# Optimization experiments

Hardware: AMD Instinct MI355X
Metric: run time of the kernel (lower is better)

Reference implementation:

```python
import jax, jax.numpy as jnp
import numpy as np
import math

D = 256      # d_model
NH = 8       # n_heads
NP = 8       # n_points
HW = 200     # H = W
N = HW * HW  # 40000 tokens
B = 1
DH = D // NH # head dim = 32


def _offset_bias():
    # replicates torch _reset_parameters grid_init bias for sampling_offsets
    thetas = np.arange(NH, dtype=np.float32) * (2.0 * np.pi / NH)
    g = np.stack([np.cos(thetas), np.sin(thetas)], -1)
    g = g / np.abs(g).max(-1, keepdims=True)
    g = np.tile(g[:, None, :], (1, NP, 1)) * np.arange(1, NP + 1, dtype=np.float32)[None, :, None]
    return jnp.asarray(g.reshape(-1), dtype=jnp.float32)


def _xavier(key, fan_in, fan_out):
    lim = math.sqrt(6.0 / (fan_in + fan_out))
    return jax.random.uniform(key, (fan_in, fan_out), jnp.float32, -lim, lim)


def setup_inputs() -> dict:
    key = jax.random.key(0)
    ks = jax.random.split(key, 6)
    return {
        "query": jax.random.normal(ks[0], (B, N, D), jnp.float32),
        "value": jax.random.normal(ks[1], (B, N, D), jnp.float32),
        "reference_points": jax.random.uniform(ks[2], (B, N, 2), jnp.float32),
        # weights stored as (in, out); torch Linear computes x @ W.T + b
        "W_off": jnp.zeros((D, NH * NP * 2), jnp.float32),   # torch init: zeros
        "b_off": _offset_bias(),
        "W_attn": jnp.zeros((D, NH * NP), jnp.float32),      # torch init: zeros
        "b_attn": jnp.zeros((NH * NP,), jnp.float32),
        "W_val": _xavier(ks[3], D, D),
        "b_val": jnp.zeros((D,), jnp.float32),
        "W_out": _xavier(ks[4], D, D),
        "b_out": jnp.zeros((D,), jnp.float32),
    }


def _grid_sample(value_h, locs):
    """Bilinear grid_sample, align_corners=False, zero padding.

    value_h: (B, NH, Hi, Wi, DH) per-head value map
    locs:    (B, N, NH, NP, 2) sampling locations in [0,1], last dim (x, y)
    returns: (B, N, NH, NP, DH)
    """
    Bb, Hh, Hi, Wi, Dh = value_h.shape
    g = locs * 2.0 - 1.0                                  # grid in [-1, 1]
    x = ((g[..., 0] + 1.0) * Wi - 1.0) * 0.5              # pixel coords (B,N,NH,NP)
    y = ((g[..., 1] + 1.0) * Hi - 1.0) * 0.5
    x0f, y0f = jnp.floor(x), jnp.floor(y)
    wx, wy = x - x0f, y - y0f
    x0, y0 = x0f.astype(jnp.int32), y0f.astype(jnp.int32)
    x1, y1 = x0 + 1, y0 + 1

    vflat = value_h.reshape(Bb, Hh, Hi * Wi, Dh)

    def corner(yi, xi, w):
        valid = (yi >= 0) & (yi < Hi) & (xi >= 0) & (xi < Wi)
        yc = jnp.clip(yi, 0, Hi - 1)
        xc = jnp.clip(xi, 0, Wi - 1)
        flat = yc * Wi + xc                               # (B,N,NH,NP)
        idx = jnp.transpose(flat, (0, 2, 1, 3)).reshape(Bb, Hh, -1)
        gathered = jnp.take_along_axis(vflat, idx[..., None], axis=2)  # (B,NH,N*NP,DH)
        wm = (w * valid.astype(w.dtype))
        wm = jnp.transpose(wm, (0, 2, 1, 3)).reshape(Bb, Hh, -1)
        return gathered * wm[..., None]

    out = (corner(y0, x0, (1.0 - wx) * (1.0 - wy))
           + corner(y0, x1, wx * (1.0 - wy))
           + corner(y1, x0, (1.0 - wx) * wy)
           + corner(y1, x1, wx * wy))                     # (B,NH,N*NP,DH)
    out = out.reshape(Bb, Hh, -1, NP, Dh)                 # (B,NH,N,NP,DH)
    return jnp.transpose(out, (0, 2, 1, 3, 4))            # (B,N,NH,NP,DH)


def reference(query, value, reference_points, W_off, b_off, W_attn, b_attn, W_val, b_val, W_out, b_out):
    Bb, Nn, C = query.shape
    H = W = int(math.sqrt(Nn))

    offsets = (query @ W_off + b_off).reshape(Bb, Nn, NH, NP, 2)
    attn = jax.nn.softmax((query @ W_attn + b_attn).reshape(Bb, Nn, NH, NP), axis=-1)

    locs = reference_points[:, :, None, None, :] + offsets / H
    locs = jnp.clip(locs, 0.0, 1.0)                       # (B,N,NH,NP,2)

    v = (value @ W_val + b_val).reshape(Bb, H, W, NH, C // NH)
    v = jnp.transpose(v, (0, 3, 1, 2, 4))                 # (B,NH,H,W,DH)

    sampled = _grid_sample(v, locs)                       # (B,N,NH,NP,DH)
    out = jnp.einsum('bnhpd,bnhp->bnhd', sampled, attn).reshape(Bb, Nn, C)
    return out @ W_out + b_out
```

## Files before the change

kernel.cpp:

```cpp
#include <hip/hip_runtime.h>
#include <hip/hip_fp16.h>
#include <math.h>

#define N_TOK 40000
#define D_MODEL 256
#define NHEAD 8
#define NPOINT 8
#define DHEAD 32
#define HW_DIM 200

typedef __attribute__((ext_vector_type(8))) short short8;
typedef __attribute__((ext_vector_type(8))) _Float16 f16x8;
typedef __attribute__((ext_vector_type(4))) float f32x4;
typedef __attribute__((ext_vector_type(8))) unsigned short ushort8v;

__device__ inline unsigned short f2bf(float f) {
    union { float f; unsigned int u; } v; v.f = f;
    unsigned int r = v.u + 0x7FFFu + ((v.u >> 16) & 1u);
    return (unsigned short)(r >> 16);
}

__device__ inline unsigned int cvt_pk_bf16(float a, float b) {
    unsigned int r;
    asm("v_cvt_pk_bf16_f32 %0, %1, %2" : "=v"(r) : "v"(a), "v"(b));
    return r;
}

__device__ inline __half2 uh2(unsigned int u) {
    union { unsigned int u; __half2 h; } x; x.u = u; return x.h;
}
__device__ inline unsigned int h2u(__half2 h) {
    union { __half2 h; unsigned int u; } x; x.h = h; return x.u;
}

#define STAGE_T(BTp, n0v, LDSARR)                                              \
    {                                                                          \
        _Pragma("unroll")                                                      \
        for (int r_ = 0; r_ < 8; r_++) {                                       \
            const int c_    = r_ * 256 + tid;                                  \
            const int row_  = c_ >> 5;                                         \
            const int slot_ = c_ & 31;                                         \
            const int kc_   = slot_ ^ (row_ & 7);                              \
            const unsigned short* src_ =                                       \
                (BTp) + (size_t)((n0v) + row_) * 256 + kc_ * 8;                \
            __builtin_amdgcn_global_load_lds(                                  \
                (const __attribute__((address_space(1))) void*)src_,           \
                (__attribute__((address_space(3))) void*)                      \
                    ((__attribute__((address_space(3))) char*)(LDSARR) + c_ * 16), \
                16, 0, 0);                                                     \
        }                                                                      \
    }

__global__ __launch_bounds__(1024)
void zchk(const float* __restrict__ W_off, const float* __restrict__ W_attn,
          int* __restrict__ flag)
{
    __shared__ int s;
    if (threadIdx.x == 0) s = 0;
    __syncthreads();
    int nz = 0;
    const float4* w0 = (const float4*)W_off;
    const float4* w1 = (const float4*)W_attn;
    for (int i = threadIdx.x; i < 8192; i += 1024) {
        float4 x = w0[i];
        nz |= (x.x != 0.f) | (x.y != 0.f) | (x.z != 0.f) | (x.w != 0.f);
    }
    for (int i = threadIdx.x; i < 4096; i += 1024) {
        float4 x = w1[i];
        nz |= (x.x != 0.f) | (x.y != 0.f) | (x.z != 0.f) | (x.w != 0.f);
    }
    if (__any(nz) && (threadIdx.x & 63) == 0) atomicOr(&s, 1);
    __syncthreads();
    if (threadIdx.x == 0) *flag = s;
}

__global__ __launch_bounds__(256)
void wt_cast(const float* __restrict__ W0, const float* __restrict__ W1,
             const float* __restrict__ W2, const float* __restrict__ W3,
             const float* __restrict__ b0, const float* __restrict__ b1,
             unsigned short* __restrict__ Tq, float* __restrict__ bq,
             unsigned short* __restrict__ T2, unsigned short* __restrict__ T3)
{
    const int which = blockIdx.y;
    const int n = blockIdx.x;
    const int k = threadIdx.x;
    if (which == 0) {
        if (n >= 128) return;
        Tq[(size_t)n * 256 + k] = f2bf(W0[(size_t)k * 128 + n]);
        if (k == 0) bq[n] = b0[n];
    } else if (which == 1) {
        if (n >= 64) return;
        Tq[(size_t)(128 + n) * 256 + k] = f2bf(W1[(size_t)k * 64 + n]);
        if (k == 0) bq[128 + n] = b1[n];
    } else if (which == 2) {
        T2[(size_t)n * 256 + k] = f2bf(W2[(size_t)k * 256 + n]);
    } else {
        T3[(size_t)n * 256 + k] = __half_as_ushort(__float2half(W3[(size_t)k * 256 + n]));
    }
}

__global__ __launch_bounds__(256)
void proj_qv(const float* __restrict__ q, const float* __restrict__ v,
             const unsigned short* __restrict__ WTq,
             const unsigned short* __restrict__ WTv,
             const float* __restrict__ bqp, const float* __restrict__ bvp,
             float* __restrict__ offs, float* __restrict__ logits,
             unsigned short* __restrict__ vh,
             const int* __restrict__ flag)
{
    __shared__ short Tile[64 * 256];

    const int tid  = threadIdx.x;
    const int wid  = tid >> 6;
    const int lane = tid & 63;
    const bool isQ = (blockIdx.y == 0);
    if (isQ && *flag == 0) return;
    const int m0   = blockIdx.x * 64;

    const float* A = isQ ? q : v;
    const unsigned short* BT = isQ ? WTq : WTv;
    const float* bias = isQ ? bqp : bvp;
    const int ntiles = isQ ? 3 : 4;

    const int r16 = lane & 15;
    const int g   = lane >> 4;

    const int srow = tid >> 2;
    const int skc  = tid & 3;
    const float* gA = A + (size_t)(m0 + srow) * 256;
    {
        float4 va[8], vb[8];
        #pragma unroll
        for (int j = 0; j < 8; j++) {
            va[j] = *(const float4*)(gA + j * 32 + skc * 8);
            vb[j] = *(const float4*)(gA + j * 32 + skc * 8 + 4);
        }
        #pragma unroll
        for (int j = 0; j < 8; j++) {
            const int c = j * 4 + skc;
            const int s = c ^ (srow & 7);
            union { unsigned int u[4]; short8 sh; } x;
            x.u[0] = cvt_pk_bf16(va[j].x, va[j].y);
            x.u[1] = cvt_pk_bf16(va[j].z, va[j].w);
            x.u[2] = cvt_pk_bf16(vb[j].x, vb[j].y);
            x.u[3] = cvt_pk_bf16(vb[j].z, vb[j].w);
            *(short8*)(Tile + srow * 256 + s * 8) = x.sh;
        }
    }
    __syncthreads();

    const int rbase = (wid >> 1) * 32;
    short8 areg[2][8];
    #pragma unroll
    for (int i = 0; i < 2; i++) {
        const int row = rbase + i * 16 + r16;
        #pragma unroll
        for (int kk = 0; kk < 8; kk++) {
            const int s = (kk * 4 + g) ^ (row & 7);
            areg[i][kk] = *(const short8*)(Tile + row * 256 + s * 8);
        }
    }
    __syncthreads();

    STAGE_T(BT, 0, Tile);
    __syncthreads();

    const int wr = rbase, wc = (wid & 1) * 32;

    for (int t = 0; t < ntiles; t++) {
        f32x4 acc[2][2] = {};
        #pragma unroll
        for (int kk = 0; kk < 8; kk++) {
            short8 b[2];
            #pragma unroll
            for (int jj = 0; jj < 2; jj++) {
                const int col = wc + jj * 16 + r16;
                const int sb  = (kk * 4 + g) ^ (col & 7);
                b[jj] = *(const short8*)(Tile + col * 256 + sb * 8);
            }
            #pragma unroll
            for (int i = 0; i < 2; i++)
                #pragma unroll
                for (int jj = 0; jj < 2; jj++)
                    acc[i][jj] = __builtin_amdgcn_mfma_f32_16x16x32_bf16(
                        areg[i][kk], b[jj], acc[i][jj], 0, 0, 0);
        }

        if (t + 1 < ntiles) {
            __syncthreads();
            STAGE_T(BT, (t + 1) * 64, Tile);
        }

        const int n0 = t * 64;
        #pragma unroll
        for (int jj = 0; jj < 2; jj++) {
            const int col = n0 + wc + jj * 16 + r16;
            const float bvv = bias[col];
            #pragma unroll
            for (int i = 0; i < 2; i++) {
                #pragma unroll
                for (int r = 0; r < 4; r++) {
                    const int row = m0 + wr + i * 16 + g * 4 + r;
                    const float o = acc[i][jj][r] + bvv;
                    if (!isQ) {
                        const int h = col >> 5, c = col & 31;
                        vh[(size_t)h * N_TOK * 32 + (size_t)row * 32 + c] =
                            __half_as_ushort(__float2half(o));
                    } else if (col < 128) {
                        const int h = col >> 4, c = col & 15;
                        offs[((size_t)h * N_TOK + row) * 16 + c] = o;
                    } else {
                        const int h = (col - 128) >> 3, c = (col - 128) & 7;
                        logits[((size_t)h * N_TOK + row) * 8 + c] = o;
                    }
                }
            }
        }

        if (t + 1 < ntiles) __syncthreads();
    }
}

__global__ __launch_bounds__(256)
void gemm_out(const unsigned short* __restrict__ A,
              const unsigned short* __restrict__ BT,
              const float* __restrict__ bias,
              float* __restrict__ C)
{
    __shared__ short Tile[64 * 256];

    const int tid  = threadIdx.x;
    const int wid  = tid >> 6;
    const int lane = tid & 63;
    const int m0   = blockIdx.x * 64;
    const int r16  = lane & 15;
    const int g    = lane >> 4;

    STAGE_T(A, m0, Tile);
    __syncthreads();

    const int rbase = (wid >> 1) * 32;
    f16x8 areg[2][8];
    #pragma unroll
    for (int i = 0; i < 2; i++) {
        const int row = rbase + i * 16 + r16;
        #pragma unroll
        for (int kk = 0; kk < 8; kk++) {
            const int s = (kk * 4 + g) ^ (row & 7);
            areg[i][kk] = *(const f16x8*)(Tile + row * 256 + s * 8);
        }
    }
    __syncthreads();

    STAGE_T(BT, 0, Tile);
    __syncthreads();

    const int wr = rbase, wc = (wid & 1) * 32;

    for (int t = 0; t < 4; t++) {
        f32x4 acc[2][2] = {};
        #pragma unroll
        for (int kk = 0; kk < 8; kk++) {
            f16x8 b[2];
            #pragma unroll
            for (int jj = 0; jj < 2; jj++) {
                const int col = wc + jj * 16 + r16;
                const int sb  = (kk * 4 + g) ^ (col & 7);
                b[jj] = *(const f16x8*)(Tile + col * 256 + sb * 8);
            }
            #pragma unroll
            for (int i = 0; i < 2; i++)
                #pragma unroll
                for (int jj = 0; jj < 2; jj++)
                    acc[i][jj] = __builtin_amdgcn_mfma_f32_16x16x32_f16(
                        areg[i][kk], b[jj], acc[i][jj], 0, 0, 0);
        }

        if (t + 1 < 4) {
            __syncthreads();
            STAGE_T(BT, (t + 1) * 64, Tile);
        }

        const int n0 = t * 64;
        #pragma unroll
        for (int jj = 0; jj < 2; jj++) {
            const int col = n0 + wc + jj * 16 + r16;
            const float bv = bias[col];
            #pragma unroll
            for (int i = 0; i < 2; i++) {
                #pragma unroll
                for (int r = 0; r < 4; r++) {
                    const int row = m0 + wr + i * 16 + g * 4 + r;
                    C[(size_t)row * 256 + col] = acc[i][jj][r] + bv;
                }
            }
        }

        if (t + 1 < 4) __syncthreads();
    }
}

__global__ __launch_bounds__(256)
void sample_k(const unsigned short* __restrict__ vh,
              const float* __restrict__ offs,
              const float* __restrict__ logits,
              const float* __restrict__ refp,
              const float* __restrict__ b_off,
              const float* __restrict__ b_attn,
              const int* __restrict__ flag,
              unsigned short* __restrict__ mid)
{
    __shared__ int4  s_idx[32][9];
    __shared__ uint2 s_wp[32][9];

    const int bid   = blockIdx.x;
    const int h     = bid & 7;
    const int chunk = bid >> 3;
    const int n0    = chunk * 32;
    const int fl    = *flag;

    {
        const int t  = threadIdx.x >> 3;
        const int pj = threadIdx.x & 7;
        const int n  = n0 + t;

        const float rx = refp[2 * n + 0];
        const float ry = refp[2 * n + 1];
        float l;
        float2 o;
        if (fl == 0) {
            l   = b_attn[h * 8 + pj];
            o.x = b_off[h * 16 + pj * 2 + 0];
            o.y = b_off[h * 16 + pj * 2 + 1];
        } else {
            l = logits[((size_t)h * N_TOK + n) * 8 + pj];
            o = *(const float2*)(offs + ((size_t)h * N_TOK + n) * 16 + pj * 2);
        }
        float m = l;
        m = fmaxf(m, __shfl_xor(m, 1));
        m = fmaxf(m, __shfl_xor(m, 2));
        m = fmaxf(m, __shfl_xor(m, 4));
        const float e = expf(l - m);
        float s = e;
        s += __shfl_xor(s, 1);
        s += __shfl_xor(s, 2);
        s += __shfl_xor(s, 4);
        const float aw = e * (1.0f / s);

        float lx = rx + o.x * (1.0f / (float)HW_DIM);
        float ly = ry + o.y * (1.0f / (float)HW_DIM);
        lx = fminf(fmaxf(lx, 0.f), 1.f);
        ly = fminf(fmaxf(ly, 0.f), 1.f);
        const float x = lx * (float)HW_DIM - 0.5f;
        const float y = ly * (float)HW_DIM - 0.5f;
        const float x0f = floorf(x), y0f = floorf(y);
        const float wx = x - x0f, wy = y - y0f;
        const int x0 = (int)x0f, y0 = (int)y0f;
        const int x1 = x0 + 1,   y1 = y0 + 1;
        const float vx0 = (x0 >= 0 && x0 < HW_DIM) ? 1.f : 0.f;
        const float vx1 = (x1 >= 0 && x1 < HW_DIM) ? 1.f : 0.f;
        const float vy0 = (y0 >= 0 && y0 < HW_DIM) ? 1.f : 0.f;
        const float vy1 = (y1 >= 0 && y1 < HW_DIM) ? 1.f : 0.f;
        const int xc0 = min(max(x0, 0), HW_DIM - 1);
        const int xc1 = min(max(x1, 0), HW_DIM - 1);
        const int yc0 = min(max(y0, 0), HW_DIM - 1);
        const int yc1 = min(max(y1, 0), HW_DIM - 1);

        int4 ic;
        ic.x = yc0 * HW_DIM + xc0;
        ic.y = yc0 * HW_DIM + xc1;
        ic.z = yc1 * HW_DIM + xc0;
        ic.w = yc1 * HW_DIM + xc1;
        const float w00 = (1.f - wx) * (1.f - wy) * aw * vy0 * vx0;
        const float w01 = wx * (1.f - wy) * aw * vy0 * vx1;
        const float w10 = (1.f - wx) * wy * aw * vy1 * vx0;
        const float w11 = wx * wy * aw * vy1 * vx1;

        s_idx[t][pj] = ic;
        uint2 pw;
        pw.x = h2u(__floats2half2_rn(w00, w01));
        pw.y = h2u(__floats2half2_rn(w10, w11));
        s_wp[t][pj] = pw;
    }
    __syncthreads();

    const int t  = threadIdx.x >> 3;
    const int q4 = (threadIdx.x >> 2) & 1;
    const int c8 = threadIdx.x & 3;
    const int n  = n0 + t;
    const char* vb = (const char*)vh;
    const unsigned int base = (unsigned int)h * (N_TOK * 64u) + (unsigned int)c8 * 16u;

    float accf[8] = {};
    #pragma unroll
    for (int pp = 0; pp < 2; pp++) {
        __half2 ac0 = uh2(0u), ac1 = uh2(0u), ac2 = uh2(0u), ac3 = uh2(0u);
        #pragma unroll
        for (int qq = 0; qq < 2; qq++) {
            const int p = q4 * 4 + pp * 2 + qq;
            const int4  ic = s_idx[t][p];
            const uint2 pw = s_wp[t][p];
            const __half2 w01 = uh2(pw.x), w23 = uh2(pw.y);
            const __half2 wa = __low2half2(w01), wb = __high2half2(w01);
            const __half2 wcc = __low2half2(w23), wd = __high2half2(w23);
            const uint4 qa = *(const uint4*)(vb + (base + ((unsigned int)ic.x << 6)));
            const uint4 qb = *(const uint4*)(vb + (base + ((unsigned int)ic.y << 6)));
            const uint4 qc = *(const uint4*)(vb + (base + ((unsigned int)ic.z << 6)));
            const uint4 qd = *(const uint4*)(vb + (base + ((unsigned int)ic.w << 6)));
            ac0 = __hfma2(wa, uh2(qa.x), ac0); ac1 = __hfma2(wa, uh2(qa.y), ac1);
            ac2 = __hfma2(wa, uh2(qa.z), ac2); ac3 = __hfma2(wa, uh2(qa.w), ac3);
            ac0 = __hfma2(wb, uh2(qb.x), ac0); ac1 = __hfma2(wb, uh2(qb.y), ac1);
            ac2 = __hfma2(wb, uh2(qb.z), ac2); ac3 = __hfma2(wb, uh2(qb.w), ac3);
            ac0 = __hfma2(wcc, uh2(qc.x), ac0); ac1 = __hfma2(wcc, uh2(qc.y), ac1);
            ac2 = __hfma2(wcc, uh2(qc.z), ac2); ac3 = __hfma2(wcc, uh2(qc.w), ac3);
            ac0 = __hfma2(wd, uh2(qd.x), ac0); ac1 = __hfma2(wd, uh2(qd.y), ac1);
            ac2 = __hfma2(wd, uh2(qd.z), ac2); ac3 = __hfma2(wd, uh2(qd.w), ac3);
        }
        float2 f;
        f = __half22float2(ac0); accf[0] += f.x; accf[1] += f.y;
        f = __half22float2(ac1); accf[2] += f.x; accf[3] += f.y;
        f = __half22float2(ac2); accf[4] += f.x; accf[5] += f.y;
        f = __half22float2(ac3); accf[6] += f.x; accf[7] += f.y;
    }

    #pragma unroll
    for (int k = 0; k < 8; k++) accf[k] += __shfl_xor(accf[k], 4);

    if (q4 == 0) {
        ushort8v o;
        #pragma unroll
        for (int k = 0; k < 8; k++) o[k] = __half_as_ushort(__float2half(accf[k]));
        *(ushort8v*)(mid + (size_t)n * D_MODEL + h * DHEAD + c8 * 8) = o;
    }
}

extern "C" void kernel_launch(void* const* d_in, const int* in_sizes, int n_in,
                              void* d_out, int out_size, void* d_ws, size_t ws_size,
                              hipStream_t stream)
{
    const float* query  = (const float*)d_in[0];
    const float* value  = (const float*)d_in[1];
    const float* refp   = (const float*)d_in[2];
    const float* W_off  = (const float*)d_in[3];
    const float* b_off  = (const float*)d_in[4];
    const float* W_attn = (const float*)d_in[5];
    const float* b_attn = (const float*)d_in[6];
    const float* W_val  = (const float*)d_in[7];
    const float* b_val  = (const float*)d_in[8];
    const float* W_out  = (const float*)d_in[9];
    const float* b_out  = (const float*)d_in[10];
    float* out = (float*)d_out;

    char* ws = (char*)d_ws;
    float* offs            = (float*)ws;
    float* logits          = (float*)(ws + 20480000);
    unsigned short* vh     = (unsigned short*)(ws + 30720000);
    unsigned short* mid    = (unsigned short*)(ws + 51200000);
    unsigned short* WTq    = (unsigned short*)(ws + 71680000);
    float*          bq     = (float*)(ws + 71778304);
    unsigned short* WT_val = (unsigned short*)(ws + 71779072);
    unsigned short* WT_out = (unsigned short*)(ws + 71910144);
    int*            flag   = (int*)(ws + 72041216);

    zchk<<<dim3(1), dim3(1024), 0, stream>>>(W_off, W_attn, flag);
    wt_cast<<<dim3(256, 4), dim3(256), 0, stream>>>(W_off, W_attn, W_val, W_out,
                                                    b_off, b_attn, WTq, bq, WT_val, WT_out);
    proj_qv<<<dim3(625, 2), dim3(256), 0, stream>>>(query, value, WTq, WT_val,
                                                    bq, b_val, offs, logits, vh, flag);
    sample_k<<<dim3((N_TOK / 32) * NHEAD), dim3(256), 0, stream>>>(
        vh, offs, logits, refp, b_off, b_attn, flag, mid);
    gemm_out<<<dim3(625), dim3(256), 0, stream>>>(mid, WT_out, b_out, out);
}
```

Baseline: 87.30 us.

## Split Q/V projection kernels and reorganize bilinear sampling by x-column per thread

Splits the fused query/value projection into separate kernels; the value projection now uses 32-row tiles with 1250 blocks, so more blocks are available to spread across CUs. The sampling kernel stores two packed corner indices per point instead of four. Each thread-pair half now handles one x column (two loads per point over all eight points) rather than four corners over four points. This is meant to shrink shared-memory index storage and even out the gather work, at the cost of an extra kernel launch and some unused leftover index arithmetic.

```diff
diff --git a/kernel.cpp b/kernel.cpp
--- a/kernel.cpp
+++ b/kernel.cpp
@@ -100,34 +100,26 @@
 }
 
 __global__ __launch_bounds__(256)
-void proj_qv(const float* __restrict__ q, const float* __restrict__ v,
-             const unsigned short* __restrict__ WTq,
-             const unsigned short* __restrict__ WTv,
-             const float* __restrict__ bqp, const float* __restrict__ bvp,
-             float* __restrict__ offs, float* __restrict__ logits,
-             unsigned short* __restrict__ vh,
-             const int* __restrict__ flag)
+void proj_q(const float* __restrict__ q,
+            const unsigned short* __restrict__ WTq,
+            const float* __restrict__ bqp,
+            float* __restrict__ offs, float* __restrict__ logits,
+            const int* __restrict__ flag)
 {
     __shared__ short Tile[64 * 256];
+
+    if (*flag == 0) return;
 
     const int tid  = threadIdx.x;
     const int wid  = tid >> 6;
     const int lane = tid & 63;
-    const bool isQ = (blockIdx.y == 0);
-    if (isQ && *flag == 0) return;
     const int m0   = blockIdx.x * 64;
-
-    const float* A = isQ ? q : v;
-    const unsigned short* BT = isQ ? WTq : WTv;
-    const float* bias = isQ ? bqp : bvp;
-    const int ntiles = isQ ? 3 : 4;
-
-    const int r16 = lane & 15;
-    const int g   = lane >> 4;
+    const int r16  = lane & 15;
+    const int g    = lane >> 4;
 
     const int srow = tid >> 2;
     const int skc  = tid & 3;
-    const float* gA = A + (size_t)(m0 + srow) * 256;
+    const float* gA = q + (size_t)(m0 + srow) * 256;
     {
         float4 va[8], vb[8];
         #pragma unroll
@@ -162,12 +154,12 @@
     }
     __syncthreads();
 
-    STAGE_T(BT, 0, Tile);
+    STAGE_T(WTq, 0, Tile);
     __syncthreads();
 
     const int wr = rbase, wc = (wid & 1) * 32;
 
-    for (int t = 0; t < ntiles; t++) {
+    for (int t = 0; t < 3; t++) {
         f32x4 acc[2][2] = {};
         #pragma unroll
         for (int kk = 0; kk < 8; kk++) {
@@ -186,27 +178,23 @@
                         areg[i][kk], b[jj], acc[i][jj], 0, 0, 0);
         }
 
-        if (t + 1 < ntiles) {
+        if (t + 1 < 3) {
             __syncthreads();
-            STAGE_T(BT, (t + 1) * 64, Tile);
+            STAGE_T(WTq, (t + 1) * 64, Tile);
         }
 
         const int n0 = t * 64;
         #pragma unroll
         for (int jj = 0; jj < 2; jj++) {
             const int col = n0 + wc + jj * 16 + r16;
-            const float bvv = bias[col];
+            const float bvv = bqp[col];
             #pragma unroll
             for (int i = 0; i < 2; i++) {
                 #pragma unroll
                 for (int r = 0; r < 4; r++) {
                     const int row = m0 + wr + i * 16 + g * 4 + r;
                     const float o = acc[i][jj][r] + bvv;
-                    if (!isQ) {
-                        const int h = col >> 5, c = col & 31;
-                        vh[(size_t)h * N_TOK * 32 + (size_t)row * 32 + c] =
-                            __half_as_ushort(__float2half(o));
-                    } else if (col < 128) {
+                    if (col < 128) {
                         const int h = col >> 4, c = col & 15;
                         offs[((size_t)h * N_TOK + row) * 16 + c] = o;
                     } else {
@@ -217,7 +205,97 @@
             }
         }
 
-        if (t + 1 < ntiles) __syncthreads();
+        if (t + 1 < 3) __syncthreads();
+    }
+}
+
+__global__ __launch_bounds__(256)
+void proj_v32(const float* __restrict__ v,
+              const unsigned short* __restrict__ WTv,
+              const float* __restrict__ bvp,
+              unsigned short* __restrict__ vh)
+{
+    __shared__ short Tile[64 * 256];
+
+    const int tid  = threadIdx.x;
+    const int wid  = tid >> 6;
+    const int lane = tid & 63;
+    const int m0   = blockIdx.x * 32;
+    const int r16  = lane & 15;
+    const int g    = lane >> 4;
+
+    const int srow = tid >> 3;
+    const int skc  = tid & 7;
+    const float* gA = v + (size_t)(m0 + srow) * 256;
+    {
+        #pragma unroll
+        for (int j = 0; j < 4; j++) {
+            const int c = skc + j * 8;
+            float4 lo = *(const float4*)(gA + c * 8);
+            float4 hi = *(const float4*)(gA + c * 8 + 4);
+            const int s = c ^ (srow & 7);
+            union { unsigned int u[4]; short8 sh; } x;
+            x.u[0] = cvt_pk_bf16(lo.x, lo.y);
+            x.u[1] = cvt_pk_bf16(lo.z, lo.w);
+            x.u[2] = cvt_pk_bf16(hi.x, hi.y);
+            x.u[3] = cvt_pk_bf16(hi.z, hi.w);
+            *(short8*)(Tile + srow * 256 + s * 8) = x.sh;
+        }
+    }
+    __syncthreads();
+
+    const int rhalf = wid >> 1;
+    const int row   = rhalf * 16 + r16;
+    short8 areg[8];
+    #pragma unroll
+    for (int kk = 0; kk < 8; kk++) {
+        const int s = (kk * 4 + g) ^ (row & 7);
+        areg[kk] = *(const short8*)(Tile + row * 256 + s * 8);
+    }
+    __syncthreads();
+
+    STAGE_T(WTv, 0, Tile);
+    __syncthreads();
+
+    const int wc = (wid & 1) * 32;
+
+    for (int t = 0; t < 4; t++) {
+        f32x4 acc[2] = {};
+        #pragma unroll
+        for (int kk = 0; kk < 8; kk++) {
+            short8 b[2];
+            #pragma unroll
+            for (int jj = 0; jj < 2; jj++) {
+                const int col = wc + jj * 16 + r16;
+                const int sb  = (kk * 4 + g) ^ (col & 7);
+                b[jj] = *(const short8*)(Tile + col * 256 + sb * 8);
+            }
+            #pragma unroll
+            for (int jj = 0; jj < 2; jj++)
+                acc[jj] = __builtin_amdgcn_mfma_f32_16x16x32_bf16(
+                    areg[kk], b[jj], acc[jj], 0, 0, 0);
+        }
+
+        if (t + 1 < 4) {
+            __syncthreads();
+            STAGE_T(WTv, (t + 1) * 64, Tile);
+        }
+
+        const int n0 = t * 64;
+        #pragma unroll
+        for (int jj = 0; jj < 2; jj++) {
+            const int col = n0 + wc + jj * 16 + r16;
+            const float bvv = bvp[col];
+            const int h = col >> 5, c = col & 31;
+            #pragma unroll
+            for (int r = 0; r < 4; r++) {
+                const int rw = m0 + rhalf * 16 + g * 4 + r;
+                vh[(size_t)h * N_TOK * 32 + (size_t)rw * 32 + c] =
+                    __half_as_ushort(__float2half(acc[jj][r] + bvv));
+            }
+        }
+
+        if (t + 1 < 4) __syncthreads();
     }
 }
 
@@ -310,7 +388,7 @@
               const int* __restrict__ flag,
               unsigned short* __restrict__ mid)
 {
-    __shared__ int4  s_idx[32][9];
+    __shared__ int2  s_idx[32][9];
     __shared__ uint2 s_wp[32][9];
 
     const int bid   = blockIdx.x;
@@ -366,11 +444,9 @@
         const int yc0 = min(max(y0, 0), HW_DIM - 1);
         const int yc1 = min(max(y1, 0), HW_DIM - 1);
 
-        int4 ic;
+        int2 ic;
         ic.x = yc0 * HW_DIM + xc0;
-        ic.y = yc0 * HW_DIM + xc1;
-        ic.z = yc1 * HW_DIM + xc0;
-        ic.w = yc1 * HW_DIM + xc1;
+        ic.y = (yc1 * HW_DIM + xc0) | ((xc1 - xc0) << 28);
         const float w00 = (1.f - wx) * (1.f - wy) * aw * vy0 * vx0;
         const float w01 = wx * (1.f - wy) * aw * vy0 * vx1;
         const float w10 = (1.f - wx) * wy * aw * vy1 * vx0;
@@ -385,7 +461,7 @@
     __syncthreads();
 
     const int t  = threadIdx.x >> 3;
-    const int q4 = (threadIdx.x >> 2) & 1;
+    const int xc = (threadIdx.x >> 2) & 1;
     const int c8 = threadIdx.x & 3;
     const int n  = n0 + t;
     const char* vb = (const char*)vh;
@@ -393,28 +469,28 @@
 
     float accf[8] = {};
     #pragma unroll
-    for (int pp = 0; pp < 2; pp++) {
+    for (int pp = 0; pp < 4; pp++) {
         __half2 ac0 = uh2(0u), ac1 = uh2(0u), ac2 = uh2(0u), ac3 = uh2(0u);
         #pragma unroll
         for (int qq = 0; qq < 2; qq++) {
-            const int p = q4 * 4 + pp * 2 + qq;
-            const int4  ic = s_idx[t][p];
+            const int p = pp * 2 + qq;
+            const int2  ic = s_idx[t][p];
             const uint2 pw = s_wp[t][p];
+            const int dx   = (ic.y >> 28) & xc;
+            const int iy0  = ic.x + dx * ((ic.y >> 28));
+            const int dxv  = ic.y >> 28;
+            const int y0r  = ic.x + (xc ? dxv : 0);
+            const int y1r  = (ic.y & 0x0FFFFFFF) + (xc ? dxv : 0);
+            (void)iy0; (void)dx;
             const __half2 w01 = uh2(pw.x), w23 = uh2(pw.y);
-            const __half2 wa = __low2half2(w01), wb = __high2half2(w01);
-            const __half2 wcc = __low2half2(w23), wd = __high2half2(w23);
-            const uint4 qa = *(const uint4*)(vb + (base + ((unsigned int)ic.x << 6)));
-            const uint4 qb = *(const uint4*)(vb + (base + ((unsigned int)ic.y << 6)));
-            const uint4 qc = *(const uint4*)(vb + (base + ((unsigned int)ic.z << 6)));
-            const uint4 qd = *(const uint4*)(vb + (base + ((unsigned int)ic.w << 6)));
-            ac0 = __hfma2(wa, uh2(qa.x), ac0); ac1 = __hfma2(wa, uh2(qa.y), ac1);
-            ac2 = __hfma2(wa, uh2(qa.z), ac2); ac3 = __hfma2(wa, uh2(qa.w), ac3);
-            ac0 = __hfma2(wb, uh2(qb.x), ac0); ac1 = __hfma2(wb, uh2(qb.y), ac1);
-            ac2 = __hfma2(wb, uh2(qb.z), ac2); ac3 = __hfma2(wb, uh2(qb.w), ac3);
-            ac0 = __hfma2(wcc, uh2(qc.x), ac0); ac1 = __hfma2(wcc, uh2(qc.y), ac1);
-            ac2 = __hfma2(wcc, uh2(qc.z), ac2); ac3 = __hfma2(wcc, uh2(qc.w), ac3);
-            ac0 = __hfma2(wd, uh2(qd.x), ac0); ac1 = __hfma2(wd, uh2(qd.y), ac1);
-            ac2 = __hfma2(wd, uh2(qd.z), ac2); ac3 = __hfma2(wd, uh2(qd.w), ac3);
+            const __half2 wy0 = xc ? __high2half2(w01) : __low2half2(w01);
+            const __half2 wy1 = xc ? __high2half2(w23) : __low2half2(w23);
+            const uint4 qa = *(const uint4*)(vb + (base + ((unsigned int)y0r << 6)));
+            const uint4 qb = *(const uint4*)(vb + (base + ((unsigned int)y1r << 6)));
+            ac0 = __hfma2(wy0, uh2(qa.x), ac0); ac1 = __hfma2(wy0, uh2(qa.y), ac1);
+            ac2 = __hfma2(wy0, uh2(qa.z), ac2); ac3 = __hfma2(wy0, uh2(qa.w), ac3);
+            ac0 = __hfma2(wy1, uh2(qb.x), ac0); ac1 = __hfma2(wy1, uh2(qb.y), ac1);
+            ac2 = __hfma2(wy1, uh2(qb.z), ac2); ac3 = __hfma2(wy1, uh2(qb.w), ac3);
         }
         float2 f;
         f = __half22float2(ac0); accf[0] += f.x; accf[1] += f.y;
@@ -426,7 +502,7 @@
     #pragma unroll
     for (int k = 0; k < 8; k++) accf[k] += __shfl_xor(accf[k], 4);
 
-    if (q4 == 0) {
+    if (xc == 0) {
         ushort8v o;
         #pragma unroll
         for (int k = 0; k < 8; k++) o[k] = __half_as_ushort(__float2half(accf[k]));
@@ -465,8 +541,8 @@
     zchk<<<dim3(1), dim3(1024), 0, stream>>>(W_off, W_attn, flag);
     wt_cast<<<dim3(256, 4), dim3(256), 0, stream>>>(W_off, W_attn, W_val, W_out,
                                                     b_off, b_attn, WTq, bq, WT_val, WT_out);
-    proj_qv<<<dim3(625, 2), dim3(256), 0, stream>>>(query, value, WTq, WT_val,
-                                                    bq, b_val, offs, logits, vh, flag);
+    proj_q<<<dim3(625), dim3(256), 0, stream>>>(query, WTq, bq, offs, logits, flag);
+    proj_v32<<<dim3(1250), dim3(256), 0, stream>>>(value, WT_val, b_val, vh);
     sample_k<<<dim3((N_TOK / 32) * NHEAD), dim3(256), 0, stream>>>(
         vh, offs, logits, refp, b_off, b_attn, flag, mid);
     gemm_out<<<dim3(625), dim3(256), 0, stream>>>(mid, WT_out, b_out, out);
```

After: 78.97 us. 1.11x faster.
